# Optimization experiments

Measured on AMD Instinct MI355X. Metric: run time of the kernel, lower is better.

Reference implementation:

```python
import jax, jax.numpy as jnp
from jax import lax
import numpy as np

STRIDE = 16
PRE_NMS = 2000
POST_NMS = 300
NMS_THRESH = 0.7
MIN_SIZE = 16.0  # * img_scale (=1.0)
DN = ('NCHW', 'OIHW', 'NCHW')


def _anchor_base(base=16, ratios=(0.5, 1.0, 2.0), scales=(8, 16, 32)):
    py = px = base / 2.0
    ab = np.zeros((len(ratios) * len(scales), 4), np.float32)
    k = 0
    for r in ratios:
        for s in scales:
            h = base * s * np.sqrt(r)
            w = base * s * np.sqrt(1.0 / r)
            ab[k] = [py - h / 2, px - w / 2, py + h / 2, px + w / 2]
            k += 1
    return ab


def _all_anchors(H, W, img_h, img_w):
    base = _anchor_base()
    sy = np.arange(H, dtype=np.float32) * STRIDE
    sx = np.arange(W, dtype=np.float32) * STRIDE
    yy, xx = np.meshgrid(sy, sx, indexing='ij')
    shifts = np.stack([yy, xx, yy, xx], axis=-1).reshape(-1, 1, 4)
    anchors = (shifts + base[None]).reshape(-1, 4).astype(np.float32)  # (H*W*9, 4)
    valid = np.where((anchors[:, 0] >= 0) & (anchors[:, 1] >= 0) &
                     (anchors[:, 2] <= img_h) & (anchors[:, 3] <= img_w))[0]
    return anchors, valid


def _loc2bbox(anc, loc):
    # anc: (1,K,4), loc: (B,K,4); boxes as (y1,x1,y2,x2)
    h = anc[..., 2] - anc[..., 0]
    w = anc[..., 3] - anc[..., 1]
    cy = anc[..., 0] + 0.5 * h
    cx = anc[..., 1] + 0.5 * w
    ncy = loc[..., 0] * h + cy
    ncx = loc[..., 1] * w + cx
    nh = h * jnp.exp(loc[..., 2])
    nw = w * jnp.exp(loc[..., 3])
    return jnp.stack([ncy - 0.5 * nh, ncx - 0.5 * nw,
                      ncy + 0.5 * nh, ncx + 0.5 * nw], axis=-1)


def _nms(boxes, scores):
    # boxes: (N,4), scores: (N,) -> (POST_NMS,4) zero-padded rois
    areas = (boxes[:, 2] - boxes[:, 0]) * (boxes[:, 3] - boxes[:, 1])

    def step(s, _):
        i = jnp.argmax(s)
        ok = s[i] > -jnp.inf
        b = boxes[i]
        yy1 = jnp.maximum(b[0], boxes[:, 0])
        xx1 = jnp.maximum(b[1], boxes[:, 1])
        yy2 = jnp.minimum(b[2], boxes[:, 2])
        xx2 = jnp.minimum(b[3], boxes[:, 3])
        inter = jnp.maximum(yy2 - yy1, 0.0) * jnp.maximum(xx2 - xx1, 0.0)
        iou = inter / (areas[i] + areas - inter + 1e-9)
        s = jnp.where(iou > NMS_THRESH, -jnp.inf, s).at[i].set(-jnp.inf)
        return s, (i, ok)

    _, (idx, ok) = lax.scan(step, scores, None, length=POST_NMS)
    return boxes[idx] * ok[:, None].astype(boxes.dtype)


def _conv(x, w, b, padding):
    y = lax.conv_general_dilated(x, w, (1, 1), padding, dimension_numbers=DN)
    return y + b[None, :, None, None]


def setup_inputs():
    key = jax.random.key(0)
    k = jax.random.split(key, 4)
    B, C, H, W = 2, 512, 64, 64
    std = 0.01
    return {
        'feat': jax.random.normal(k[0], (B, C, H, W), jnp.float32),
        'share_w': jax.random.normal(k[1], (512, 512, 3, 3), jnp.float32) * std,
        'share_b': jnp.zeros((512,), jnp.float32),
        'cls_w': jax.random.normal(k[2], (18, 512, 1, 1), jnp.float32) * std,
        'cls_b': jnp.zeros((18,), jnp.float32),
        'reg_w': jax.random.normal(k[3], (36, 512, 1, 1), jnp.float32) * std,
        'reg_b': jnp.zeros((36,), jnp.float32),
        'img_h': 1024,
        'img_w': 1024,
    }


def reference(feat, share_w, share_b, cls_w, cls_b, reg_w, reg_b, img_h, img_w):
    B, _, H, W = feat.shape
    anchors_np, valid_np = _all_anchors(H, W, img_h, img_w)
    anchors = jnp.asarray(anchors_np)
    valid = jnp.asarray(valid_np)

    shared = jax.nn.relu(_conv(feat, share_w, share_b, 'SAME'))
    cls = _conv(shared, cls_w, cls_b, 'VALID')   # (B,18,H,W)
    reg = _conv(shared, reg_w, reg_b, 'VALID')   # (B,36,H,W)

    # permute(0,2,3,1).view(-1,2), gather valid anchors, softmax
    cls = cls.transpose(0, 2, 3, 1).reshape(B, -1, 2)[:, valid]   # (B,K,2)
    cls = jax.nn.softmax(cls, axis=-1)
    reg = reg.transpose(0, 2, 3, 1).reshape(B, -1, 4)[:, valid]   # (B,K,4)

    # proposal layer: decode, clip, min-size filter, top-k, NMS
    anc = anchors[valid][None]                                    # (1,K,4)
    boxes = _loc2bbox(anc, reg)                                   # (B,K,4)
    boxes = jnp.stack([jnp.clip(boxes[..., 0], 0.0, img_h),
                       jnp.clip(boxes[..., 1], 0.0, img_w),
                       jnp.clip(boxes[..., 2], 0.0, img_h),
                       jnp.clip(boxes[..., 3], 0.0, img_w)], axis=-1)
    hs = boxes[..., 2] - boxes[..., 0]
    ws = boxes[..., 3] - boxes[..., 1]
    scores = jnp.where((hs >= MIN_SIZE) & (ws >= MIN_SIZE), cls[..., 1], -jnp.inf)

    top_s, top_i = lax.top_k(scores, PRE_NMS)                     # (B,PRE_NMS)
    top_boxes = jnp.take_along_axis(boxes, top_i[..., None], axis=1)
    rois = jax.vmap(_nms)(top_boxes, top_s)                       # (B,POST_NMS,4)
    roi_list = rois.reshape(-1, 4)
    roi_id = jnp.repeat(jnp.arange(B, dtype=jnp.int32), POST_NMS)
    return cls, reg, roi_list, roi_id, anchors
```

## Files before the change

### kernel.cpp

```cpp
#include <hip/hip_runtime.h>
#include <math.h>

typedef unsigned int u32;
typedef unsigned long long u64;
typedef unsigned short ushort_t;

typedef __attribute__((ext_vector_type(8))) short short8;
typedef __attribute__((ext_vector_type(4))) float f32x4;

template <int N> struct Ic { static constexpr int value = N; };

#define KANC 18376
#define PRE 2000
#define PREP 2048
#define POST 300

#define OUT_CLS 0
#define OUT_REG 73504
#define OUT_ROI 220512
#define OUT_RID 222912
#define OUT_ANC 223512

#define WS_NHWC   0u
#define WS_FT     16777216u
#define WS_W3     41943040u
#define WS_VPOS   56098816u
#define WS_BOXES  56246272u
#define WS_KEYS   56834304u
#define WS_TOPBOX 56981312u
#define WS_TOPKEY 57046848u
#define WS_MASK   57063232u

#define A_SPL2 7920

__device__ __forceinline__ ushort_t f2bf(float f) {
    u32 u = __float_as_uint(f);
    u32 r = (u + 0x7FFFu + ((u >> 16) & 1u)) >> 16;
    return (ushort_t)r;
}
__device__ __forceinline__ float bf2f(ushort_t h) {
    return __uint_as_float(((u32)h) << 16);
}

__device__ __forceinline__ void anchor_base(int t, float& y1, float& x1, float& y2, float& x2) {
    const double ratios[3] = {0.5, 1.0, 2.0};
    const double scales[3] = {8.0, 16.0, 32.0};
    double r = ratios[t / 3], s = scales[t % 3];
    double h = 16.0 * s * sqrt(r);
    double w = 16.0 * s * sqrt(1.0 / r);
    y1 = (float)(8.0 - h * 0.5);
    x1 = (float)(8.0 - w * 0.5);
    y2 = (float)(8.0 + h * 0.5);
    x2 = (float)(8.0 + w * 0.5);
}

__global__ __launch_bounds__(256) void t1_feat(const float* __restrict__ feat,
                                               ushort_t* __restrict__ ft) {
    int by = blockIdx.y;
    int b = by >> 6, y = by & 63;
    int ci0 = blockIdx.x * 64;
    int tid = threadIdx.x;
    __shared__ float tile[64 * 65];
    for (int it = 0; it < 16; it++) {
        int idx = it * 256 + tid;
        int ci = idx >> 6, x = idx & 63;
        tile[ci * 65 + x] = feat[((size_t)(b * 512 + ci0 + ci) * 64 + y) * 64 + x];
    }
    __syncthreads();
    for (int it = 0; it < 16; it++) {
        int idx = it * 256 + tid;
        int x = idx >> 6, ci = idx & 63;
        float v = tile[ci * 65 + x];
        ushort_t hi = f2bf(v);
        float r1 = v - bf2f(hi);
        ushort_t mid = f2bf(r1);
        float r2 = r1 - bf2f(mid);
        ushort_t lo = f2bf(r2);
        size_t base = ((size_t)(b * 64 + y) * 64 + x) * 512 + ci0 + ci;
        const size_t spl = (size_t)2 * 64 * 64 * 512;
        ft[base] = hi;
        ft[base + spl] = mid;
        ft[base + 2 * spl] = lo;
    }
}

__global__ __launch_bounds__(256) void t2_wgt(const float* __restrict__ w,
                                              ushort_t* __restrict__ w3) {
    int tg = blockIdx.x * 256 + threadIdx.x;
    int co = tg >> 9, ci = tg & 511;
    const size_t spl = (size_t)9 * 512 * 512;
    for (int kk = 0; kk < 9; kk++) {
        float v = w[(size_t)(co * 512 + ci) * 9 + kk];
        ushort_t hi = f2bf(v);
        float r1 = v - bf2f(hi);
        ushort_t mid = f2bf(r1);
        float r2 = r1 - bf2f(mid);
        ushort_t lo = f2bf(r2);
        size_t base = ((size_t)kk * 512 + co) * 512 + ci;
        w3[base] = hi;
        w3[base + spl] = mid;
        w3[base + 2 * spl] = lo;
    }
}

__global__ __launch_bounds__(1024) void k0_anchors(float* out, int* vpos,
                                                   const int* d_imgh, const int* d_imgw) {
    int tid = threadIdx.x;
    float imgh = (float)d_imgh[0], imgw = (float)d_imgw[0];
    __shared__ int cnt[1024];
    int base = tid * 36;
    int c = 0;
    for (int k = 0; k < 36; k++) {
        int a = base + k;
        int t = a % 9; int pix = a / 9; int x = pix & 63; int y = pix >> 6;
        float b0, b1, b2, b3; anchor_base(t, b0, b1, b2, b3);
        float a0 = b0 + 16.0f * y, a1 = b1 + 16.0f * x;
        float a2 = b2 + 16.0f * y, a3 = b3 + 16.0f * x;
        out[OUT_ANC + a * 4 + 0] = a0;
        out[OUT_ANC + a * 4 + 1] = a1;
        out[OUT_ANC + a * 4 + 2] = a2;
        out[OUT_ANC + a * 4 + 3] = a3;
        if (a0 >= 0.0f && a1 >= 0.0f && a2 <= imgh && a3 <= imgw) c++;
    }
    cnt[tid] = c;
    __syncthreads();
    for (int off = 1; off < 1024; off <<= 1) {
        int v = cnt[tid];
        int u = (tid >= off) ? cnt[tid - off] : 0;
        __syncthreads();
        cnt[tid] = v + u;
        __syncthreads();
    }
    int j = (tid == 0) ? 0 : cnt[tid - 1];
    for (int k = 0; k < 36; k++) {
        int a = base + k;
        int t = a % 9; int pix = a / 9; int x = pix & 63; int y = pix >> 6;
        float b0, b1, b2, b3; anchor_base(t, b0, b1, b2, b3);
        float a0 = b0 + 16.0f * y, a1 = b1 + 16.0f * x;
        float a2 = b2 + 16.0f * y, a3 = b3 + 16.0f * x;
        bool ok = (a0 >= 0.0f && a1 >= 0.0f && a2 <= imgh && a3 <= imgw);
        vpos[a] = ok ? j : -1;
        if (ok) j++;
    }
}

__global__ __launch_bounds__(256, 2) void k1_conv(const ushort_t* __restrict__ ft,
                                                  const ushort_t* __restrict__ w3,
                                                  const float* __restrict__ bias,
                                                  float* __restrict__ nhwc) {
    __shared__ ushort_t lds16[3 * A_SPL2];
    int tid = threadIdx.x;
    int bid = blockIdx.x;
    int nt = (bid >> 1) & 3;
    int mt = ((bid >> 3) << 1) | (bid & 1);
    int b = mt >> 6, y = mt & 63;
    int nb = nt << 7;

    int lane = tid & 63;
    int w = tid >> 6;
    int wn = w << 5;
    int mlane = lane & 15;
    int quad = lane >> 4;
    int koff8 = quad * 8;

    const size_t FT_SPL = (size_t)2 * 64 * 64 * 512;
    const size_t W3_SPL = (size_t)9 * 512 * 512;

    int sx = tid >> 2;
    int sq = tid & 3;

    f32x4 acc[4][2];
#pragma unroll
    for (int mi = 0; mi < 4; mi++)
#pragma unroll
        for (int ni = 0; ni < 2; ni++) {
            acc[mi][ni][0] = 0.f; acc[mi][ni][1] = 0.f;
            acc[mi][ni][2] = 0.f; acc[mi][ni][3] = 0.f;
        }

    float bv[2];
#pragma unroll
    for (int ni = 0; ni < 2; ni++) bv[ni] = bias[nb + wn + ni * 16 + mlane];

    if (tid < 72) {
        int s = tid / 24, rem = tid % 24;
        int r = rem >> 3, rem2 = rem & 7;
        int side = rem2 >> 2, q = rem2 & 3;
        uint4 z = make_uint4(0, 0, 0, 0);
        *(uint4*)&lds16[s * A_SPL2 + (r * 66 + side * 65) * 40 + q * 8] = z;
    }

    uint4 pbA[9];
    auto loadA = [&](int ct) {
#pragma unroll
        for (int r = 0; r < 3; r++) {
            int yy = y - 1 + r;
            bool valid = (yy >= 0 && yy < 64);
            size_t rowbase = ((size_t)(b * 64 + (valid ? yy : 0)) * 64 + sx) * 512 + ct * 32 + sq * 8;
#pragma unroll
            for (int s = 0; s < 3; s++) {
                uint4 v = make_uint4(0, 0, 0, 0);
                if (valid) v = *(const uint4*)&ft[rowbase + (size_t)s * FT_SPL];
                pbA[r * 3 + s] = v;
            }
        }
    };
    auto writeA = [&]() {
#pragma unroll
        for (int r = 0; r < 3; r++)
#pragma unroll
            for (int s = 0; s < 3; s++)
                *(uint4*)&lds16[s * A_SPL2 + (r * 66 + sx + 1) * 40 + sq * 8] = pbA[r * 3 + s];
    };

    short8 breg[2][2][3];
    auto loadB = [&](int buf, int tap, int ct) {
#pragma unroll
        for (int ni = 0; ni < 2; ni++) {
            size_t cobase = ((size_t)(tap * 512 + nb + wn + ni * 16 + mlane)) * 512 + ct * 32 + koff8;
#pragma unroll
            for (int s = 0; s < 3; s++)
                breg[buf][ni][s] = *(const short8*)&w3[(size_t)s * W3_SPL + cobase];
        }
    };

    auto ct_body = [&](int ct, auto par_c) {
        constexpr int PAR = decltype(par_c)::value;
        __syncthreads();
        writeA();
        __syncthreads();
        if (ct < 15) loadA(ct + 1);

#pragma unroll
        for (int tap = 0; tap < 9; tap++) {
            int cur = (tap + PAR) & 1, alt = cur ^ 1;
            if (tap < 8) loadB(alt, tap + 1, ct);
            else if (ct < 15) loadB(alt, 0, ct + 1);
            int ky = tap / 3, kx = tap - ky * 3;

            short8 af[3][4];
#pragma unroll
            for (int s = 0; s < 3; s++) {
                int ab = s * A_SPL2 + (ky * 66 + mlane + kx) * 40 + koff8;
#pragma unroll
                for (int mi = 0; mi < 4; mi++)
                    af[s][mi] = *(const short8*)&lds16[ab + mi * 640];
            }
#pragma unroll
            for (int t = 0; t < 6; t++) {
                const int sa_t[6] = {0, 0, 1, 0, 1, 2};
                const int sb_t[6] = {0, 1, 0, 2, 1, 0};
                int sa = sa_t[t], sb = sb_t[t];
#pragma unroll
                for (int mi = 0; mi < 4; mi++)
#pragma unroll
                    for (int ni = 0; ni < 2; ni++)
                        acc[mi][ni] = __builtin_amdgcn_mfma_f32_16x16x32_bf16(
                            af[sa][mi], breg[cur][ni][sb], acc[mi][ni], 0, 0, 0);
            }
        }
    };

    loadA(0);
    loadB(0, 0, 0);

    for (int ct = 0; ct < 16; ct += 2) {
        ct_body(ct, Ic<0>{});
        ct_body(ct + 1, Ic<1>{});
    }

#pragma unroll
    for (int mi = 0; mi < 4; mi++) {
#pragma unroll
        for (int r = 0; r < 4; r++) {
            int x = mi * 16 + quad * 4 + r;
            size_t obase = ((size_t)(b * 64 + y) * 64 + x) * 512;
#pragma unroll
            for (int ni = 0; ni < 2; ni++) {
                int co = nb + wn + ni * 16 + mlane;
                float v = acc[mi][ni][r] + bv[ni];
                nhwc[obase + co] = fmaxf(v, 0.0f);
            }
        }
    }
}

__global__ __launch_bounds__(256) void k2_heads(const float* __restrict__ nhwc,
                                                const float* __restrict__ cls_w,
                                                const float* __restrict__ cls_b,
                                                const float* __restrict__ reg_w,
                                                const float* __restrict__ reg_b,
                                                const int* __restrict__ vpos,
                                                float* __restrict__ out,
                                                float* __restrict__ boxes_ws,
                                                u32* __restrict__ keys_ws,
                                                const int* d_imgh, const int* d_imgw) {
    int row = blockIdx.x;
    int b = row >> 6, y = row & 63;
    int tid = threadIdx.x;
    __shared__ float Al[64 * 65];
    __shared__ float Wl[54 * 64];
    __shared__ float Ob[54 * 64];
    int p = tid & 63, g = tid >> 6;
    int o0 = g * 14;
    int no = (g == 3) ? 12 : 14;
    float acc[14];
#pragma unroll
    for (int i = 0; i < 14; i++) acc[i] = 0.0f;
    for (int cib = 0; cib < 512; cib += 64) {
        for (int s = tid; s < 4096; s += 256) {
            int kk = s & 63, pp = s >> 6;
            Al[pp * 65 + kk] = nhwc[((size_t)(b * 64 + y) * 64 + pp) * 512 + cib + kk];
        }
        for (int s = tid; s < 54 * 64; s += 256) {
            int o = s >> 6, kk = s & 63;
            Wl[s] = (o < 18) ? cls_w[o * 512 + cib + kk] : reg_w[(o - 18) * 512 + cib + kk];
        }
        __syncthreads();
        for (int kk = 0; kk < 64; kk++) {
            float a = Al[p * 65 + kk];
#pragma unroll
            for (int oo = 0; oo < 14; oo++)
                if (oo < no) acc[oo] += a * Wl[(o0 + oo) * 64 + kk];
        }
        __syncthreads();
    }
#pragma unroll
    for (int oo = 0; oo < 14; oo++)
        if (oo < no) {
            int o = o0 + oo;
            float bvv = (o < 18) ? cls_b[o] : reg_b[o - 18];
            Ob[o * 64 + p] = acc[oo] + bvv;
        }
    __syncthreads();
    float imgh = (float)d_imgh[0], imgw = (float)d_imgw[0];
    for (int task = tid; task < 576; task += 256) {
        int ta = task >> 6, p2 = task & 63;
        int a_idx = (y * 64 + p2) * 9 + ta;
        int j = vpos[a_idx];
        if (j < 0) continue;
        float c0 = Ob[(2 * ta) * 64 + p2], c1 = Ob[(2 * ta + 1) * 64 + p2];
        float m = fmaxf(c0, c1);
        float e0 = expf(c0 - m), e1 = expf(c1 - m);
        float sden = e0 + e1;
        float p0v = e0 / sden, p1v = e1 / sden;
        out[OUT_CLS + (size_t)(b * KANC + j) * 2 + 0] = p0v;
        out[OUT_CLS + (size_t)(b * KANC + j) * 2 + 1] = p1v;
        float l0 = Ob[(18 + 4 * ta + 0) * 64 + p2];
        float l1 = Ob[(18 + 4 * ta + 1) * 64 + p2];
        float l2 = Ob[(18 + 4 * ta + 2) * 64 + p2];
        float l3 = Ob[(18 + 4 * ta + 3) * 64 + p2];
        out[OUT_REG + (size_t)(b * KANC + j) * 4 + 0] = l0;
        out[OUT_REG + (size_t)(b * KANC + j) * 4 + 1] = l1;
        out[OUT_REG + (size_t)(b * KANC + j) * 4 + 2] = l2;
        out[OUT_REG + (size_t)(b * KANC + j) * 4 + 3] = l3;
        float b0, b1, b2, b3; anchor_base(ta, b0, b1, b2, b3);
        float ay1 = b0 + 16.0f * y, ax1 = b1 + 16.0f * p2;
        float ay2 = b2 + 16.0f * y, ax2 = b3 + 16.0f * p2;
        float h = ay2 - ay1, wdt = ax2 - ax1;
        float cy = ay1 + 0.5f * h, cx = ax1 + 0.5f * wdt;
        float ncy = l0 * h + cy, ncx = l1 * wdt + cx;
        float nh = h * expf(l2), nw = wdt * expf(l3);
        float by1 = fminf(fmaxf(ncy - 0.5f * nh, 0.0f), imgh);
        float bx1 = fminf(fmaxf(ncx - 0.5f * nw, 0.0f), imgw);
        float by2 = fminf(fmaxf(ncy + 0.5f * nh, 0.0f), imgh);
        float bx2 = fminf(fmaxf(ncx + 0.5f * nw, 0.0f), imgw);
        boxes_ws[(size_t)(b * KANC + j) * 4 + 0] = by1;
        boxes_ws[(size_t)(b * KANC + j) * 4 + 1] = bx1;
        boxes_ws[(size_t)(b * KANC + j) * 4 + 2] = by2;
        boxes_ws[(size_t)(b * KANC + j) * 4 + 3] = bx2;
        float hs = by2 - by1, wsz = bx2 - bx1;
        u32 key = 0;
        if (hs >= 16.0f && wsz >= 16.0f) key = __float_as_uint(p1v) + 1u;
        keys_ws[b * KANC + j] = key;
    }
}

__device__ __forceinline__ void suffix_scan(u32* suf, const u32* hist, int N, int tid) {
    for (int i = tid; i < N; i += 1024) suf[i] = hist[i];
    if (tid == 0) suf[N] = 0;
    __syncthreads();
    for (int off = 1; off < N; off <<= 1) {
        u32 add0 = 0, add1 = 0;
        int i0 = tid, i1 = tid + 1024;
        if (i0 < N) add0 = (i0 + off < N) ? suf[i0 + off] : 0;
        if (i1 < N) add1 = (i1 + off < N) ? suf[i1 + off] : 0;
        __syncthreads();
        if (i0 < N) suf[i0] += add0;
        if (i1 < N) suf[i1] += add1;
        __syncthreads();
    }
}

__global__ __launch_bounds__(1024) void k3_select(const u32* __restrict__ keys_ws,
                                                  const float* __restrict__ boxes_ws,
                                                  u32* __restrict__ topkey,
                                                  float* __restrict__ topbox) {
    int b = blockIdx.x, tid = threadIdx.x;
    const u32* keys = keys_ws + (size_t)b * KANC;
    __shared__ u32 hist[2048];
    __shared__ u32 suf[2049];
    __shared__ int Ps;
    __shared__ int cnt;
    __shared__ u64 sbuf[4096];

    for (int i = tid; i < 2048; i += 1024) hist[i] = 0;
    __syncthreads();
    for (int i = tid; i < KANC; i += 1024) atomicAdd(&hist[keys[i] >> 20], 1u);
    __syncthreads();
    suffix_scan(suf, hist, 2048, tid);
    if (tid == 0) Ps = 0;
    __syncthreads();
    for (int i = tid; i < 2048; i += 1024)
        if (suf[i] >= (u32)PRE && suf[i + 1] < (u32)PRE) Ps = i;
    __syncthreads();
    u32 P1 = (u32)Ps;
    u32 quota2 = (u32)PRE - suf[P1 + 1];
    __syncthreads();

    for (int i = tid; i < 1024; i += 1024) hist[i] = 0;
    __syncthreads();
    for (int i = tid; i < KANC; i += 1024) {
        u32 k = keys[i];
        if ((k >> 20) == P1) atomicAdd(&hist[(k >> 10) & 1023u], 1u);
    }
    __syncthreads();
    suffix_scan(suf, hist, 1024, tid);
    if (tid == 0) Ps = 0;
    __syncthreads();
    for (int i = tid; i < 1024; i += 1024)
        if (suf[i] >= quota2 && suf[i + 1] < quota2) Ps = i;
    __syncthreads();
    u32 P2 = (u32)Ps;
    u32 quota3 = quota2 - suf[P2 + 1];
    __syncthreads();

    u32 pref = (P1 << 10) | P2;
    for (int i = tid; i < 1024; i += 1024) hist[i] = 0;
    __syncthreads();
    for (int i = tid; i < KANC; i += 1024) {
        u32 k = keys[i];
        if ((k >> 10) == pref) atomicAdd(&hist[k & 1023u], 1u);
    }
    __syncthreads();
    suffix_scan(suf, hist, 1024, tid);
    if (tid == 0) Ps = 0;
    __syncthreads();
    for (int i = tid; i < 1024; i += 1024)
        if (suf[i] >= quota3 && suf[i + 1] < quota3) Ps = i;
    __syncthreads();
    u32 P3 = (u32)Ps;
    u32 T = (P1 << 20) | (P2 << 10) | P3;
    u32 Tm = (T < 1u) ? 1u : T;

    for (int i = tid; i < 4096; i += 1024) sbuf[i] = 0ull;
    if (tid == 0) cnt = 0;
    __syncthreads();
    for (int i = tid; i < KANC; i += 1024) {
        u32 k = keys[i];
        if (k >= Tm) {
            int pos = atomicAdd(&cnt, 1);
            if (pos < 4096)
                sbuf[pos] = ((u64)k << 32) | (u64)(0xFFFFFFFFu - (u32)i);
        }
    }
    __syncthreads();

    for (int k2 = 2; k2 <= 4096; k2 <<= 1) {
        for (int j2 = k2 >> 1; j2 > 0; j2 >>= 1) {
            for (int i = tid; i < 4096; i += 1024) {
                int ixj = i ^ j2;
                if (ixj > i) {
                    u64 va = sbuf[i], vb = sbuf[ixj];
                    bool descRegion = ((i & k2) == 0);
                    if (descRegion ? (va < vb) : (va > vb)) {
                        sbuf[i] = vb; sbuf[ixj] = va;
                    }
                }
            }
            __syncthreads();
        }
    }

    for (int i = tid; i < PREP; i += 1024) {
        u64 v = sbuf[i];
        u32 kk = (u32)(v >> 32);
        u32 j = 0xFFFFFFFFu - (u32)(v & 0xFFFFFFFFull);
        bool good = (i < PRE) && (kk != 0);
        topkey[b * PREP + i] = good ? kk : 0;
        float4 bx = make_float4(0.0f, 0.0f, 0.0f, 0.0f);
        if (good) bx = *(const float4*)&boxes_ws[(size_t)(b * KANC + j) * 4];
        *(float4*)&topbox[(size_t)(b * PREP + i) * 4] = bx;
    }
}

__global__ __launch_bounds__(64) void k4_mask(const float* __restrict__ topbox,
                                              u64* __restrict__ mask) {
    int jb = blockIdx.x, ib = blockIdx.y, b = blockIdx.z;
    int lane = threadIdx.x;
    float4 bi = *(const float4*)&topbox[(size_t)(b * PREP + ib * 64 + lane) * 4];
    float4 bj = *(const float4*)&topbox[(size_t)(b * PREP + jb * 64 + lane) * 4];
    float ai = (bi.z - bi.x) * (bi.w - bi.y);
    float aj = (bj.z - bj.x) * (bj.w - bj.y);
    u64 word = 0;
    for (int ii = 0; ii < 64; ii++) {
        float y1 = __shfl(bi.x, ii), x1 = __shfl(bi.y, ii);
        float y2 = __shfl(bi.z, ii), x2 = __shfl(bi.w, ii);
        float aii = __shfl(ai, ii);
        float yy1 = fmaxf(y1, bj.x), xx1 = fmaxf(x1, bj.y);
        float yy2 = fminf(y2, bj.z), xx2 = fminf(x2, bj.w);
        float inter = fmaxf(yy2 - yy1, 0.0f) * fmaxf(xx2 - xx1, 0.0f);
        float iou = inter / (aii + aj - inter + 1e-9f);
        u64 bal = __ballot(iou > 0.7f);
        if (lane == ii) word = bal;
    }
    mask[(size_t)(b * PREP + ib * 64 + lane) * 32 + jb] = word;
}

__global__ __launch_bounds__(64) void k5_nms(const u32* __restrict__ topkey,
                                             const float* __restrict__ topbox,
                                             const u64* __restrict__ mask,
                                             float* __restrict__ out) {
    int b = blockIdx.x;
    int lane = threadIdx.x;
    __shared__ u32 keys_s[PREP];
    __shared__ int kept[POST];
    for (int s = lane; s < PREP; s += 64) keys_s[s] = topkey[b * PREP + s];
    __syncthreads();
    const u64* mb = mask + (size_t)b * PREP * 32;
    u64 remv = 0;
    const int CH = 16;
    u64 bufA[CH], bufB[CH];
    auto loadRows = [&](u64* buf, int base) {
#pragma unroll
        for (int k = 0; k < CH; k++)
            buf[k] = (lane < 32) ? mb[(size_t)(base + k) * 32 + lane] : 0ull;
    };
    int nk = 0;
    bool done = false;
    loadRows(bufA, 0);
    for (int base = 0; base < PRE && !done; base += 2 * CH) {
        loadRows(bufB, base + CH);
#pragma unroll
        for (int k = 0; k < CH; k++) {
            int i = base + k;
            u64 wv = __shfl(remv, i >> 6);
            if (!((wv >> (i & 63)) & 1ull) && keys_s[i] != 0) {
                remv |= bufA[k];
                if (lane == 0) kept[nk] = i;
                nk++;
                if (nk == POST) { done = true; break; }
            }
        }
        if (!done && base + CH < PRE) {
            if (base + 2 * CH < PRE) loadRows(bufA, base + 2 * CH);
#pragma unroll
            for (int k = 0; k < CH; k++) {
                int i = base + CH + k;
                u64 wv = __shfl(remv, i >> 6);
                if (!((wv >> (i & 63)) & 1ull) && keys_s[i] != 0) {
                    remv |= bufB[k];
                    if (lane == 0) kept[nk] = i;
                    nk++;
                    if (nk == POST) { done = true; break; }
                }
            }
        }
    }
    __syncthreads();
    for (int s = lane; s < POST; s += 64) {
        float4 bx = make_float4(0.0f, 0.0f, 0.0f, 0.0f);
        if (s < nk) bx = *(const float4*)&topbox[(size_t)(b * PREP + kept[s]) * 4];
        *(float4*)&out[OUT_ROI + (size_t)(b * POST + s) * 4] = bx;
        out[OUT_RID + b * POST + s] = (float)b;
    }
}

extern "C" void kernel_launch(void* const* d_in, const int* in_sizes, int n_in,
                              void* d_out, int out_size, void* d_ws, size_t ws_size,
                              hipStream_t stream) {
    (void)in_sizes; (void)n_in; (void)out_size; (void)ws_size;
    const float* feat    = (const float*)d_in[0];
    const float* share_w = (const float*)d_in[1];
    const float* share_b = (const float*)d_in[2];
    const float* cls_w   = (const float*)d_in[3];
    const float* cls_b   = (const float*)d_in[4];
    const float* reg_w   = (const float*)d_in[5];
    const float* reg_b   = (const float*)d_in[6];
    const int*   imgh    = (const int*)d_in[7];
    const int*   imgw    = (const int*)d_in[8];
    float* out = (float*)d_out;
    char* ws = (char*)d_ws;
    float*     nhwc   = (float*)(ws + WS_NHWC);
    ushort_t*  ft     = (ushort_t*)(ws + WS_FT);
    ushort_t*  w3     = (ushort_t*)(ws + WS_W3);
    int*       vpos   = (int*)(ws + WS_VPOS);
    float*     boxes  = (float*)(ws + WS_BOXES);
    u32*       keys   = (u32*)(ws + WS_KEYS);
    float*     topbox = (float*)(ws + WS_TOPBOX);
    u32*       topkey = (u32*)(ws + WS_TOPKEY);
    u64*       mask   = (u64*)(ws + WS_MASK);

    t1_feat<<<dim3(8, 128), 256, 0, stream>>>(feat, ft);
    t2_wgt<<<1024, 256, 0, stream>>>(share_w, w3);
    k0_anchors<<<1, 1024, 0, stream>>>(out, vpos, imgh, imgw);
    k1_conv<<<512, 256, 0, stream>>>(ft, w3, share_b, nhwc);
    k2_heads<<<128, 256, 0, stream>>>(nhwc, cls_w, cls_b, reg_w, reg_b, vpos,
                                      out, boxes, keys, imgh, imgw);
    k3_select<<<2, 1024, 0, stream>>>(keys, boxes, topkey, topbox);
    k4_mask<<<dim3(32, 32, 2), 64, 0, stream>>>(topbox, mask);
    k5_nms<<<2, 64, 0, stream>>>(topkey, topbox, mask, out);
}
```

Measured before the change: 725.8 us.

## Split-K conv with 32x32 MFMA, closed-form anchors, bitmask NMS scan, fused bias/ReLU

The main conv now uses 32x32x16 bf16 MFMA tiles and splits the 16 channel tiles into two halves across twice as many blocks. Partial sums are combined with float atomics into a zeroed buffer, and bias plus ReLU move into the heads kernel. Anchors are computed in parallel with a closed-form valid-index prefix instead of a single-block scan. The NMS scan walks candidate bits with ctz over a validity ballot, and the head dot products are vectorised. The added parallelism targets conv occupancy, at the cost of a memset and atomic traffic on a large fp32 tensor.

```diff
diff --git a/kernel.cpp b/kernel.cpp
--- a/kernel.cpp
+++ b/kernel.cpp
@@ -6,9 +6,7 @@
 typedef unsigned short ushort_t;
 
 typedef __attribute__((ext_vector_type(8))) short short8;
-typedef __attribute__((ext_vector_type(4))) float f32x4;
-
-template <int N> struct Ic { static constexpr int value = N; };
+typedef __attribute__((ext_vector_type(16))) float f32x16;
 
 #define KANC 18376
 #define PRE 2000
@@ -43,11 +41,11 @@
 }
 
 __device__ __forceinline__ void anchor_base(int t, float& y1, float& x1, float& y2, float& x2) {
-    const double ratios[3] = {0.5, 1.0, 2.0};
-    const double scales[3] = {8.0, 16.0, 32.0};
-    double r = ratios[t / 3], s = scales[t % 3];
-    double h = 16.0 * s * sqrt(r);
-    double w = 16.0 * s * sqrt(1.0 / r);
+    const double SQ[3] = {0.7071067811865476, 1.0, 1.4142135623730951};
+    const double SC[3] = {8.0, 16.0, 32.0};
+    int ri = t / 3, si = t % 3;
+    double h = 16.0 * SC[si] * SQ[ri];
+    double w = 16.0 * SC[si] * SQ[2 - ri];
     y1 = (float)(8.0 - h * 0.5);
     x1 = (float)(8.0 - w * 0.5);
     y2 = (float)(8.0 + h * 0.5);
@@ -103,65 +101,61 @@
     }
 }
 
-__global__ __launch_bounds__(1024) void k0_anchors(float* out, int* vpos,
-                                                   const int* d_imgh, const int* d_imgw) {
-    int tid = threadIdx.x;
+__global__ __launch_bounds__(256) void k0_anchors(float* out, int* vpos,
+                                                  const int* d_imgh, const int* d_imgw) {
+    int a = blockIdx.x * 256 + threadIdx.x;
     float imgh = (float)d_imgh[0], imgw = (float)d_imgw[0];
-    __shared__ int cnt[1024];
-    int base = tid * 36;
-    int c = 0;
-    for (int k = 0; k < 36; k++) {
-        int a = base + k;
-        int t = a % 9; int pix = a / 9; int x = pix & 63; int y = pix >> 6;
-        float b0, b1, b2, b3; anchor_base(t, b0, b1, b2, b3);
-        float a0 = b0 + 16.0f * y, a1 = b1 + 16.0f * x;
-        float a2 = b2 + 16.0f * y, a3 = b3 + 16.0f * x;
-        out[OUT_ANC + a * 4 + 0] = a0;
-        out[OUT_ANC + a * 4 + 1] = a1;
-        out[OUT_ANC + a * 4 + 2] = a2;
-        out[OUT_ANC + a * 4 + 3] = a3;
-        if (a0 >= 0.0f && a1 >= 0.0f && a2 <= imgh && a3 <= imgw) c++;
-    }
-    cnt[tid] = c;
-    __syncthreads();
-    for (int off = 1; off < 1024; off <<= 1) {
-        int v = cnt[tid];
-        int u = (tid >= off) ? cnt[tid - off] : 0;
-        __syncthreads();
-        cnt[tid] = v + u;
-        __syncthreads();
-    }
-    int j = (tid == 0) ? 0 : cnt[tid - 1];
-    for (int k = 0; k < 36; k++) {
-        int a = base + k;
-        int t = a % 9; int pix = a / 9; int x = pix & 63; int y = pix >> 6;
-        float b0, b1, b2, b3; anchor_base(t, b0, b1, b2, b3);
-        float a0 = b0 + 16.0f * y, a1 = b1 + 16.0f * x;
-        float a2 = b2 + 16.0f * y, a3 = b3 + 16.0f * x;
-        bool ok = (a0 >= 0.0f && a1 >= 0.0f && a2 <= imgh && a3 <= imgw);
-        vpos[a] = ok ? j : -1;
-        if (ok) j++;
-    }
-}
-
-__global__ __launch_bounds__(256, 2) void k1_conv(const ushort_t* __restrict__ ft,
+    int t = a % 9, pix = a / 9, x = pix & 63, y = pix >> 6;
+    int j = 0;
+    bool myvalid = false;
+#pragma unroll
+    for (int tt = 0; tt < 9; tt++) {
+        float c0, c1, c2, c3;
+        anchor_base(tt, c0, c1, c2, c3);
+        int ylo = (int)((-c0) / 16.0f) + 1;
+        int yhi = (int)((imgh - c2) / 16.0f);
+        int xlo = (int)((-c1) / 16.0f) + 1;
+        int xhi = (int)((imgw - c3) / 16.0f);
+        ylo = max(ylo, 0); yhi = min(yhi, 63);
+        xlo = max(xlo, 0); xhi = min(xhi, 63);
+        int Wt  = max(xhi - xlo + 1, 0);
+        int nry = max(yhi - ylo + 1, 0);
+        int rb  = min(max(y - ylo, 0), nry);
+        bool vy = (y >= ylo) && (y <= yhi);
+        int cb  = vy ? min(max(x - xlo, 0), Wt) : 0;
+        bool val = vy && (x >= xlo) && (x <= xhi);
+        j += rb * Wt + cb + ((tt < t && val) ? 1 : 0);
+        if (tt == t) {
+            myvalid = val;
+            float4 o;
+            o.x = c0 + 16.0f * y;
+            o.y = c1 + 16.0f * x;
+            o.z = c2 + 16.0f * y;
+            o.w = c3 + 16.0f * x;
+            *(float4*)&out[OUT_ANC + a * 4] = o;
+        }
+    }
+    vpos[a] = myvalid ? j : -1;
+}
+
+__global__ __launch_bounds__(256, 3) void k1_conv(const ushort_t* __restrict__ ft,
                                                   const ushort_t* __restrict__ w3,
-                                                  const float* __restrict__ bias,
                                                   float* __restrict__ nhwc) {
     __shared__ ushort_t lds16[3 * A_SPL2];
     int tid = threadIdx.x;
     int bid = blockIdx.x;
     int nt = (bid >> 1) & 3;
-    int mt = ((bid >> 3) << 1) | (bid & 1);
+    int kh = (bid >> 3) & 1;
+    int mt = ((bid >> 4) << 1) | (bid & 1);
     int b = mt >> 6, y = mt & 63;
     int nb = nt << 7;
+    int ct0 = kh * 8;
 
     int lane = tid & 63;
     int w = tid >> 6;
     int wn = w << 5;
-    int mlane = lane & 15;
-    int quad = lane >> 4;
-    int koff8 = quad * 8;
+    int nlane = lane & 31;
+    int kgrp8 = (lane >> 5) * 8;
 
     const size_t FT_SPL = (size_t)2 * 64 * 64 * 512;
     const size_t W3_SPL = (size_t)9 * 512 * 512;
@@ -169,18 +163,11 @@
     int sx = tid >> 2;
     int sq = tid & 3;
 
-    f32x4 acc[4][2];
-#pragma unroll
-    for (int mi = 0; mi < 4; mi++)
-#pragma unroll
-        for (int ni = 0; ni < 2; ni++) {
-            acc[mi][ni][0] = 0.f; acc[mi][ni][1] = 0.f;
-            acc[mi][ni][2] = 0.f; acc[mi][ni][3] = 0.f;
-        }
-
-    float bv[2];
-#pragma unroll
-    for (int ni = 0; ni < 2; ni++) bv[ni] = bias[nb + wn + ni * 16 + mlane];
+    f32x16 acc[2];
+#pragma unroll
+    for (int mi = 0; mi < 2; mi++)
+#pragma unroll
+        for (int r = 0; r < 16; r++) acc[mi][r] = 0.0f;
 
     if (tid < 72) {
         int s = tid / 24, rem = tid % 24;
@@ -213,38 +200,38 @@
                 *(uint4*)&lds16[s * A_SPL2 + (r * 66 + sx + 1) * 40 + sq * 8] = pbA[r * 3 + s];
     };
 
-    short8 breg[2][2][3];
-    auto loadB = [&](int buf, int tap, int ct) {
-#pragma unroll
-        for (int ni = 0; ni < 2; ni++) {
-            size_t cobase = ((size_t)(tap * 512 + nb + wn + ni * 16 + mlane)) * 512 + ct * 32 + koff8;
-#pragma unroll
-            for (int s = 0; s < 3; s++)
-                breg[buf][ni][s] = *(const short8*)&w3[(size_t)s * W3_SPL + cobase];
-        }
+    short8 breg[2][3];
+    auto loadB = [&](int buf, int tap, int ks, int ct) {
+        size_t cobase = ((size_t)(tap * 512 + nb + wn + nlane)) * 512 + ct * 32 + ks * 16 + kgrp8;
+#pragma unroll
+        for (int s = 0; s < 3; s++)
+            breg[buf][s] = *(const short8*)&w3[(size_t)s * W3_SPL + cobase];
     };
 
-    auto ct_body = [&](int ct, auto par_c) {
-        constexpr int PAR = decltype(par_c)::value;
+    loadA(ct0);
+    loadB(0, 0, 0, ct0);
+
+    for (int ct = ct0; ct < ct0 + 8; ct++) {
         __syncthreads();
         writeA();
         __syncthreads();
-        if (ct < 15) loadA(ct + 1);
-
-#pragma unroll
-        for (int tap = 0; tap < 9; tap++) {
-            int cur = (tap + PAR) & 1, alt = cur ^ 1;
-            if (tap < 8) loadB(alt, tap + 1, ct);
-            else if (ct < 15) loadB(alt, 0, ct + 1);
+        if (ct + 1 < ct0 + 8) loadA(ct + 1);
+
+#pragma unroll
+        for (int u = 0; u < 18; u++) {
+            int cur = u & 1, alt = cur ^ 1;
+            if (u + 1 < 18) loadB(alt, (u + 1) >> 1, (u + 1) & 1, ct);
+            else if (ct + 1 < ct0 + 8) loadB(alt, 0, 0, ct + 1);
+            int tap = u >> 1, ks = u & 1;
             int ky = tap / 3, kx = tap - ky * 3;
 
-            short8 af[3][4];
+            short8 af[3][2];
 #pragma unroll
             for (int s = 0; s < 3; s++) {
-                int ab = s * A_SPL2 + (ky * 66 + mlane + kx) * 40 + koff8;
-#pragma unroll
-                for (int mi = 0; mi < 4; mi++)
-                    af[s][mi] = *(const short8*)&lds16[ab + mi * 640];
+#pragma unroll
+                for (int mi = 0; mi < 2; mi++)
+                    af[s][mi] = *(const short8*)&lds16[s * A_SPL2 +
+                        (ky * 66 + mi * 32 + nlane + kx) * 40 + ks * 16 + kgrp8];
             }
 #pragma unroll
             for (int t = 0; t < 6; t++) {
@@ -252,40 +239,26 @@
                 const int sb_t[6] = {0, 1, 0, 2, 1, 0};
                 int sa = sa_t[t], sb = sb_t[t];
 #pragma unroll
-                for (int mi = 0; mi < 4; mi++)
-#pragma unroll
-                    for (int ni = 0; ni < 2; ni++)
-                        acc[mi][ni] = __builtin_amdgcn_mfma_f32_16x16x32_bf16(
-                            af[sa][mi], breg[cur][ni][sb], acc[mi][ni], 0, 0, 0);
+                for (int mi = 0; mi < 2; mi++)
+                    acc[mi] = __builtin_amdgcn_mfma_f32_32x32x16_bf16(
+                        af[sa][mi], breg[cur][sb], acc[mi], 0, 0, 0);
             }
         }
-    };
-
-    loadA(0);
-    loadB(0, 0, 0);
-
-    for (int ct = 0; ct < 16; ct += 2) {
-        ct_body(ct, Ic<0>{});
-        ct_body(ct + 1, Ic<1>{});
-    }
-
-#pragma unroll
-    for (int mi = 0; mi < 4; mi++) {
-#pragma unroll
-        for (int r = 0; r < 4; r++) {
-            int x = mi * 16 + quad * 4 + r;
-            size_t obase = ((size_t)(b * 64 + y) * 64 + x) * 512;
-#pragma unroll
-            for (int ni = 0; ni < 2; ni++) {
-                int co = nb + wn + ni * 16 + mlane;
-                float v = acc[mi][ni][r] + bv[ni];
-                nhwc[obase + co] = fmaxf(v, 0.0f);
-            }
+    }
+
+    int co = nb + wn + nlane;
+#pragma unroll
+    for (int mi = 0; mi < 2; mi++) {
+#pragma unroll
+        for (int r = 0; r < 16; r++) {
+            int xx = mi * 32 + (r & 3) + 8 * (r >> 2) + 4 * (lane >> 5);
+            atomicAdd(&nhwc[((size_t)(b * 64 + y) * 64 + xx) * 512 + co], acc[mi][r]);
         }
     }
 }
 
 __global__ __launch_bounds__(256) void k2_heads(const float* __restrict__ nhwc,
+                                                const float* __restrict__ share_b,
                                                 const float* __restrict__ cls_w,
                                                 const float* __restrict__ cls_b,
                                                 const float* __restrict__ reg_w,
@@ -298,7 +271,7 @@
     int row = blockIdx.x;
     int b = row >> 6, y = row & 63;
     int tid = threadIdx.x;
-    __shared__ float Al[64 * 65];
+    __shared__ float Al[64 * 68];
     __shared__ float Wl[54 * 64];
     __shared__ float Ob[54 * 64];
     int p = tid & 63, g = tid >> 6;
@@ -310,18 +283,22 @@
     for (int cib = 0; cib < 512; cib += 64) {
         for (int s = tid; s < 4096; s += 256) {
             int kk = s & 63, pp = s >> 6;
-            Al[pp * 65 + kk] = nhwc[((size_t)(b * 64 + y) * 64 + pp) * 512 + cib + kk];
+            float v = nhwc[((size_t)(b * 64 + y) * 64 + pp) * 512 + cib + kk] + share_b[cib + kk];
+            Al[pp * 68 + kk] = fmaxf(v, 0.0f);
         }
         for (int s = tid; s < 54 * 64; s += 256) {
             int o = s >> 6, kk = s & 63;
             Wl[s] = (o < 18) ? cls_w[o * 512 + cib + kk] : reg_w[(o - 18) * 512 + cib + kk];
         }
         __syncthreads();
-        for (int kk = 0; kk < 64; kk++) {
-            float a = Al[p * 65 + kk];
+        for (int kq = 0; kq < 16; kq++) {
+            float4 a4 = *(const float4*)&Al[p * 68 + kq * 4];
 #pragma unroll
             for (int oo = 0; oo < 14; oo++)
-                if (oo < no) acc[oo] += a * Wl[(o0 + oo) * 64 + kk];
+                if (oo < no) {
+                    float4 w4 = *(const float4*)&Wl[(o0 + oo) * 64 + kq * 4];
+                    acc[oo] += a4.x * w4.x + a4.y * w4.y + a4.z * w4.z + a4.w * w4.w;
+                }
         }
         __syncthreads();
     }
@@ -523,10 +500,14 @@
                                              float* __restrict__ out) {
     int b = blockIdx.x;
     int lane = threadIdx.x;
-    __shared__ u32 keys_s[PREP];
     __shared__ int kept[POST];
-    for (int s = lane; s < PREP; s += 64) keys_s[s] = topkey[b * PREP + s];
-    __syncthreads();
+
+    u64 validw = 0;
+    for (int it = 0; it < 32; it++) {
+        u64 wv = __ballot(topkey[b * PREP + it * 64 + lane] != 0);
+        if (lane == it) validw = wv;
+    }
+
     const u64* mb = mask + (size_t)b * PREP * 32;
     u64 remv = 0;
     const int CH = 16;
@@ -537,34 +518,31 @@
             buf[k] = (lane < 32) ? mb[(size_t)(base + k) * 32 + lane] : 0ull;
     };
     int nk = 0;
-    bool done = false;
+    auto process = [&](u64* buf, int base) {
+        int wi = base >> 6, sh = base & 63;
+        u64 supw = __shfl(remv, wi);
+        u64 valw = __shfl(validw, wi);
+        u32 cand = (u32)(((~supw & valw) >> sh) & 0xFFFFull);
+        while (cand) {
+            int k = __builtin_ctz(cand);
+            cand &= cand - 1;
+            int i = base + k;
+            remv |= buf[k];
+            u64 rw = __shfl(buf[k], wi);
+            cand &= ~((u32)((rw >> sh) & 0xFFFFull));
+            if (lane == 0) kept[nk] = i;
+            nk++;
+            if (nk == POST) break;
+        }
+    };
+
     loadRows(bufA, 0);
-    for (int base = 0; base < PRE && !done; base += 2 * CH) {
+    for (int base = 0; base < PRE && nk < POST; base += 2 * CH) {
         loadRows(bufB, base + CH);
-#pragma unroll
-        for (int k = 0; k < CH; k++) {
-            int i = base + k;
-            u64 wv = __shfl(remv, i >> 6);
-            if (!((wv >> (i & 63)) & 1ull) && keys_s[i] != 0) {
-                remv |= bufA[k];
-                if (lane == 0) kept[nk] = i;
-                nk++;
-                if (nk == POST) { done = true; break; }
-            }
-        }
-        if (!done && base + CH < PRE) {
+        process(bufA, base);
+        if (nk < POST && base + CH < PRE) {
             if (base + 2 * CH < PRE) loadRows(bufA, base + 2 * CH);
-#pragma unroll
-            for (int k = 0; k < CH; k++) {
-                int i = base + CH + k;
-                u64 wv = __shfl(remv, i >> 6);
-                if (!((wv >> (i & 63)) & 1ull) && keys_s[i] != 0) {
-                    remv |= bufB[k];
-                    if (lane == 0) kept[nk] = i;
-                    nk++;
-                    if (nk == POST) { done = true; break; }
-                }
-            }
+            process(bufB, base + CH);
         }
     }
     __syncthreads();
@@ -599,15 +577,16 @@
     u32*       keys   = (u32*)(ws + WS_KEYS);
     float*     topbox = (float*)(ws + WS_TOPBOX);
     u32*       topkey = (u32*)(ws + WS_TOPKEY);
-    u64*       mask   = (u64*)(ws + WS_MASK);
-
+    u64*       maskp  = (u64*)(ws + WS_MASK);
+
+    hipMemsetAsync(nhwc, 0, (size_t)2 * 64 * 64 * 512 * 4, stream);
     t1_feat<<<dim3(8, 128), 256, 0, stream>>>(feat, ft);
     t2_wgt<<<1024, 256, 0, stream>>>(share_w, w3);
-    k0_anchors<<<1, 1024, 0, stream>>>(out, vpos, imgh, imgw);
-    k1_conv<<<512, 256, 0, stream>>>(ft, w3, share_b, nhwc);
-    k2_heads<<<128, 256, 0, stream>>>(nhwc, cls_w, cls_b, reg_w, reg_b, vpos,
+    k0_anchors<<<144, 256, 0, stream>>>(out, vpos, imgh, imgw);
+    k1_conv<<<1024, 256, 0, stream>>>(ft, w3, nhwc);
+    k2_heads<<<128, 256, 0, stream>>>(nhwc, share_b, cls_w, cls_b, reg_w, reg_b, vpos,
                                       out, boxes, keys, imgh, imgw);
     k3_select<<<2, 1024, 0, stream>>>(keys, boxes, topkey, topbox);
-    k4_mask<<<dim3(32, 32, 2), 64, 0, stream>>>(topbox, mask);
-    k5_nms<<<2, 64, 0, stream>>>(topkey, topbox, mask, out);
-}
+    k4_mask<<<dim3(32, 32, 2), 64, 0, stream>>>(topbox, maskp);
+    k5_nms<<<2, 64, 0, stream>>>(topkey, topbox, maskp, out);
+}
```

Result: faster. 663.4 us (-8.6%).
